# Optimization experiments

Hardware: AMD Instinct MI355X
Metric: run time of the kernel (lower is better)

Reference implementation:

```python
import jax, jax.numpy as jnp
import numpy as np

VOCAB = 200000
EMB = 128
HID = 128
NT = 16
B = 4096


def setup_inputs() -> dict:
    key = jax.random.key(0)
    ks = jax.random.split(key, 8)
    x = jax.random.randint(ks[0], (B, 1), 0, VOCAB, dtype=jnp.int64)
    emb = jax.random.normal(ks[1], (VOCAB, EMB), dtype=jnp.float32) * 0.02
    emb = emb.at[0].set(0.0)  # padding_idx=0
    s = 1.0 / np.sqrt(HID)
    w_ih = jax.random.uniform(ks[2], (4 * HID, EMB), minval=-s, maxval=s, dtype=jnp.float32)
    w_hh = jax.random.uniform(ks[3], (4 * HID, HID), minval=-s, maxval=s, dtype=jnp.float32)
    b_ih = jax.random.uniform(ks[4], (4 * HID,), minval=-s, maxval=s, dtype=jnp.float32)
    b_hh = jax.random.uniform(ks[5], (4 * HID,), minval=-s, maxval=s, dtype=jnp.float32)
    w_fc = jax.random.uniform(ks[6], (NT, HID), minval=-s, maxval=s, dtype=jnp.float32)
    b_fc = jax.random.uniform(ks[7], (NT,), minval=-s, maxval=s, dtype=jnp.float32)
    return {"x": x, "emb": emb, "w_ih": w_ih, "w_hh": w_hh,
            "b_ih": b_ih, "b_hh": b_hh, "w_fc": w_fc, "b_fc": b_fc}


def _lstm(xs, w_ih, w_hh, b_ih, b_hh):
    # xs: [T, E]; torch LSTM with batch=1, gate order i, f, g, o
    H = HID
    b = b_ih + b_hh

    def step(carry, xt):
        h, c = carry
        z = xt @ w_ih.T + h @ w_hh.T + b  # [4H]
        i = jax.nn.sigmoid(z[:H])
        f = jax.nn.sigmoid(z[H:2 * H])
        g = jnp.tanh(z[2 * H:3 * H])
        o = jax.nn.sigmoid(z[3 * H:])
        c = f * c + i * g
        h = o * jnp.tanh(c)
        return (h, c), h

    init = (jnp.zeros((H,), xs.dtype), jnp.zeros((H,), xs.dtype))
    _, hs = jax.lax.scan(step, init, xs)
    return hs  # [T, H]


def reference(x, emb, w_ih, w_hh, b_ih, b_hh, w_fc, b_fc):
    emb = emb.at[0].set(0.0)  # padding_idx=0
    xe = emb[x[:, 0]]  # [B, E] == lstm input viewed as (seq=B, batch=1, E)
    hs = _lstm(xe, w_ih, w_hh, b_ih, b_hh)  # [B, H]
    out = hs @ w_fc.T + b_fc  # [B, NT]; torch .squeeze(1) is a no-op for NT>1
    return out
```

## Files before the change

### kernel.cpp

```cpp
#include <hip/hip_runtime.h>
#include <math.h>

#define EMBD 128
#define HIDD 128
#define NTAR 16
#define BSEQ 4096
#define G4   512
#define CH   8

typedef _Float16 v2h __attribute__((ext_vector_type(2)));

#define DPP_ADD(x, ctrl)                                                     \
    ((x) + __int_as_float(__builtin_amdgcn_update_dpp(                       \
               0, __float_as_int(x), (ctrl), 0xf, 0xf, true)))

__device__ __forceinline__ float fast_sigmoid(float z) {
    return __builtin_amdgcn_rcpf(1.f + __expf(-z));
}
__device__ __forceinline__ float fast_tanh(float z) {
    return 1.f - 2.f * __builtin_amdgcn_rcpf(1.f + __expf(2.f * z));
}

__device__ __forceinline__ v2h pack_f16(float f0, float f1) {
    return __builtin_bit_cast(v2h, __builtin_amdgcn_cvt_pkrtz(f0, f1));
}

__global__ void input_proj_kernel(const int* __restrict__ x,
                                  const float* __restrict__ emb,
                                  const float* __restrict__ w_ih,
                                  const float* __restrict__ b_ih,
                                  const float* __restrict__ b_hh,
                                  float* __restrict__ zxT) {
    const int t = blockIdx.x;
    const int j = threadIdx.x;
    const int u = j >> 2;
    const int g = j & 3;
    const int row = g * HIDD + u;
    const int idx = x[t];
    const float4* __restrict__ er = (const float4*)(emb + (long long)idx * EMBD);
    const float4* __restrict__ wr = (const float4*)(w_ih + row * EMBD);
    float acc = 0.f;
#pragma unroll
    for (int k = 0; k < EMBD / 4; ++k) {
        float4 e = er[k];
        float4 w = wr[k];
        acc += e.x * w.x + e.y * w.y + e.z * w.z + e.w * w.w;
    }
    zxT[(t * HIDD + u) * 4 + g] = acc + b_ih[row] + b_hh[row];
}

__global__ __launch_bounds__(512, 2)
void lstm_seq_kernel(const float* __restrict__ zxT,
                     const float* __restrict__ w_hh,
                     float* __restrict__ hs) {
    __shared__ __align__(16) _Float16 h_db[2][HIDD];

    const int tid = threadIdx.x;
    const int l   = tid & 63;
    const int wv  = tid >> 6;
    const int kq  = l & 3;
    const int us  = l >> 2;
    const int u   = wv * 16 + us;
    const bool writer = (kq == 0);

    v2h w2h[4][16];
#pragma unroll
    for (int g = 0; g < 4; ++g) {
        const float* __restrict__ wr = w_hh + (g * HIDD + u) * HIDD + 32 * kq;
#pragma unroll
        for (int j = 0; j < 4; ++j) {
            const int c0 = 8 * ((j + kq) & 3);
#pragma unroll
            for (int p = 0; p < 4; ++p) {
                const float f0 = wr[c0 + 2 * p];
                const float f1 = wr[c0 + 2 * p + 1];
                w2h[g][4 * j + p] = pack_f16(f0, f1);
            }
        }
    }
#pragma unroll
    for (int g = 0; g < 4; ++g)
#pragma unroll
        for (int k = 0; k < 16; ++k)
            asm volatile("" : "+v"(w2h[g][k]));

    if (tid < HIDD) {
        h_db[0][tid] = (_Float16)0.f;
        h_db[1][tid] = (_Float16)0.f;
    }
    float c = 0.f;
    float hreg[CH];
    float4 zcur[CH];
#pragma unroll
    for (int s = 0; s < CH; ++s) hreg[s] = 0.f;

    const float4* __restrict__ zx4 = (const float4*)zxT;
    __syncthreads();

    for (int tc = 0; tc < BSEQ; tc += CH) {
        if (writer && tc > 0) {
#pragma unroll
            for (int s = 0; s < CH; ++s)
                hs[(tc - CH + s) * HIDD + u] = hreg[s];
        }
#pragma unroll
        for (int s = 0; s < CH; ++s)
            zcur[s] = zx4[(tc + s) * HIDD + u];

#pragma unroll
        for (int s = 0; s < CH; ++s) {
            const uint4* __restrict__ rb =
                (const uint4*)(&h_db[s & 1][32 * kq]);
            const int wb = (s & 1) ^ 1;

            float z0 = 0.f, z1 = 0.f, z2 = 0.f, z3 = 0.f;
#pragma unroll
            for (int j = 0; j < 4; ++j) {
                const int cj = (j + kq) & 3;
                const uint4 hb = rb[cj];
                v2h hp[4];
                hp[0] = __builtin_bit_cast(v2h, hb.x);
                hp[1] = __builtin_bit_cast(v2h, hb.y);
                hp[2] = __builtin_bit_cast(v2h, hb.z);
                hp[3] = __builtin_bit_cast(v2h, hb.w);
#pragma unroll
                for (int p = 0; p < 4; ++p) {
                    z0 = __builtin_amdgcn_fdot2(hp[p], w2h[0][4 * j + p], z0, false);
                    z1 = __builtin_amdgcn_fdot2(hp[p], w2h[1][4 * j + p], z1, false);
                    z2 = __builtin_amdgcn_fdot2(hp[p], w2h[2][4 * j + p], z2, false);
                    z3 = __builtin_amdgcn_fdot2(hp[p], w2h[3][4 * j + p], z3, false);
                }
            }

            z0 = DPP_ADD(z0, 0xB1); z0 = DPP_ADD(z0, 0x4E);
            z1 = DPP_ADD(z1, 0xB1); z1 = DPP_ADD(z1, 0x4E);
            z2 = DPP_ADD(z2, 0xB1); z2 = DPP_ADD(z2, 0x4E);
            z3 = DPP_ADD(z3, 0xB1); z3 = DPP_ADD(z3, 0x4E);

            const float4 zb = zcur[s];
            const float gi = fast_sigmoid(z0 + zb.x);
            const float gf = fast_sigmoid(z1 + zb.y);
            const float gg = fast_tanh   (z2 + zb.z);
            const float go = fast_sigmoid(z3 + zb.w);
            c = gf * c + gi * gg;
            const float h = go * fast_tanh(c);
            hreg[s] = h;
            if (writer) h_db[wb][u] = (_Float16)h;
            __syncthreads();
        }
    }
    if (writer) {
#pragma unroll
        for (int s = 0; s < CH; ++s)
            hs[(BSEQ - CH + s) * HIDD + u] = hreg[s];
    }
}

__global__ void fc_kernel(const float* __restrict__ hs,
                          const float* __restrict__ w_fc,
                          const float* __restrict__ b_fc,
                          float* __restrict__ out) {
    const int gid = blockIdx.x * blockDim.x + threadIdx.x;
    if (gid >= BSEQ * NTAR) return;
    const int n = gid & (NTAR - 1);
    const int t = gid >> 4;
    const float4* __restrict__ hr = (const float4*)(hs + t * HIDD);
    const float4* __restrict__ wr = (const float4*)(w_fc + n * HIDD);
    float acc = 0.f;
#pragma unroll
    for (int k = 0; k < HIDD / 4; ++k) {
        float4 h = hr[k];
        float4 wv = wr[k];
        acc += h.x * wv.x + h.y * wv.y + h.z * wv.z + h.w * wv.w;
    }
    out[gid] = acc + b_fc[n];
}

extern "C" void kernel_launch(void* const* d_in, const int* in_sizes, int n_in,
                              void* d_out, int out_size, void* d_ws, size_t ws_size,
                              hipStream_t stream) {
    const int*   x    = (const int*)d_in[0];
    const float* emb  = (const float*)d_in[1];
    const float* w_ih = (const float*)d_in[2];
    const float* w_hh = (const float*)d_in[3];
    const float* b_ih = (const float*)d_in[4];
    const float* b_hh = (const float*)d_in[5];
    const float* w_fc = (const float*)d_in[6];
    const float* b_fc = (const float*)d_in[7];
    float* out = (float*)d_out;

    float* zxT = (float*)d_ws;
    float* hs  = zxT + (size_t)BSEQ * G4;

    input_proj_kernel<<<BSEQ, G4, 0, stream>>>(x, emb, w_ih, b_ih, b_hh, zxT);
    lstm_seq_kernel<<<1, 512, 0, stream>>>(zxT, w_hh, hs);
    fc_kernel<<<(BSEQ * NTAR + 255) / 256, 256, 0, stream>>>(hs, w_fc, b_fc, out);
}
```

Before: 2.439 ms.

## Distribute gate activations across quad lanes, prefetch next input chunk, split accumulators

Each of the four lanes in a quad now evaluates a single gate activation, selected per lane, using one exp and one rcp with per-lane constants so sigmoid and tanh share a formula. The four results are then broadcast to every lane of the quad with DPP. Input-projection values are loaded as one scalar per lane and prefetched one chunk ahead to hide global load latency in the serial loop. The fdot2 accumulation chains are split into two halves to shorten dependency chains, at the cost of extra selects, DPP moves and registers.

```diff
diff --git a/kernel.cpp b/kernel.cpp
--- a/kernel.cpp
+++ b/kernel.cpp
@@ -13,10 +13,10 @@
 #define DPP_ADD(x, ctrl)                                                     \
     ((x) + __int_as_float(__builtin_amdgcn_update_dpp(                       \
                0, __float_as_int(x), (ctrl), 0xf, 0xf, true)))
-
-__device__ __forceinline__ float fast_sigmoid(float z) {
-    return __builtin_amdgcn_rcpf(1.f + __expf(-z));
-}
+#define DPP_BCAST(x, ctrl)                                                   \
+    (__int_as_float(__builtin_amdgcn_update_dpp(                             \
+         0, __float_as_int(x), (ctrl), 0xf, 0xf, true)))
+
 __device__ __forceinline__ float fast_tanh(float z) {
     return 1.f - 2.f * __builtin_amdgcn_rcpf(1.f + __expf(2.f * z));
 }
@@ -63,6 +63,10 @@
     const int u   = wv * 16 + us;
     const bool writer = (kq == 0);
 
+    const float mA = (kq == 2) ? 2.f : -1.f;
+    const float cA = (kq == 2) ? -2.f : 1.f;
+    const float cB = (kq == 2) ? 1.f : 0.f;
+
     v2h w2h[4][16];
 #pragma unroll
     for (int g = 0; g < 4; ++g) {
@@ -90,11 +94,13 @@
     }
     float c = 0.f;
     float hreg[CH];
-    float4 zcur[CH];
-#pragma unroll
-    for (int s = 0; s < CH; ++s) hreg[s] = 0.f;
-
-    const float4* __restrict__ zx4 = (const float4*)zxT;
+    float zcur[CH], zfut[CH];
+    const int zoff = wv * 64 + l;
+#pragma unroll
+    for (int s = 0; s < CH; ++s) {
+        zcur[s] = zxT[s * G4 + zoff];
+        hreg[s] = 0.f;
+    }
     __syncthreads();
 
     for (int tc = 0; tc < BSEQ; tc += CH) {
@@ -103,9 +109,12 @@
             for (int s = 0; s < CH; ++s)
                 hs[(tc - CH + s) * HIDD + u] = hreg[s];
         }
-#pragma unroll
-        for (int s = 0; s < CH; ++s)
-            zcur[s] = zx4[(tc + s) * HIDD + u];
+        {
+            const int tn = (tc + CH < BSEQ) ? (tc + CH) : (BSEQ - CH);
+#pragma unroll
+            for (int s = 0; s < CH; ++s)
+                zfut[s] = zxT[(tn + s) * G4 + zoff];
+        }
 
 #pragma unroll
         for (int s = 0; s < CH; ++s) {
@@ -113,7 +122,8 @@
                 (const uint4*)(&h_db[s & 1][32 * kq]);
             const int wb = (s & 1) ^ 1;
 
-            float z0 = 0.f, z1 = 0.f, z2 = 0.f, z3 = 0.f;
+            float z0a = 0.f, z1a = 0.f, z2a = 0.f, z3a = 0.f;
+            float z0b = 0.f, z1b = 0.f, z2b = 0.f, z3b = 0.f;
 #pragma unroll
             for (int j = 0; j < 4; ++j) {
                 const int cj = (j + kq) & 3;
@@ -123,31 +133,53 @@
                 hp[1] = __builtin_bit_cast(v2h, hb.y);
                 hp[2] = __builtin_bit_cast(v2h, hb.z);
                 hp[3] = __builtin_bit_cast(v2h, hb.w);
-#pragma unroll
-                for (int p = 0; p < 4; ++p) {
-                    z0 = __builtin_amdgcn_fdot2(hp[p], w2h[0][4 * j + p], z0, false);
-                    z1 = __builtin_amdgcn_fdot2(hp[p], w2h[1][4 * j + p], z1, false);
-                    z2 = __builtin_amdgcn_fdot2(hp[p], w2h[2][4 * j + p], z2, false);
-                    z3 = __builtin_amdgcn_fdot2(hp[p], w2h[3][4 * j + p], z3, false);
+                if (j < 2) {
+#pragma unroll
+                    for (int p = 0; p < 4; ++p) {
+                        z0a = __builtin_amdgcn_fdot2(hp[p], w2h[0][4 * j + p], z0a, false);
+                        z1a = __builtin_amdgcn_fdot2(hp[p], w2h[1][4 * j + p], z1a, false);
+                        z2a = __builtin_amdgcn_fdot2(hp[p], w2h[2][4 * j + p], z2a, false);
+                        z3a = __builtin_amdgcn_fdot2(hp[p], w2h[3][4 * j + p], z3a, false);
+                    }
+                } else {
+#pragma unroll
+                    for (int p = 0; p < 4; ++p) {
+                        z0b = __builtin_amdgcn_fdot2(hp[p], w2h[0][4 * j + p], z0b, false);
+                        z1b = __builtin_amdgcn_fdot2(hp[p], w2h[1][4 * j + p], z1b, false);
+                        z2b = __builtin_amdgcn_fdot2(hp[p], w2h[2][4 * j + p], z2b, false);
+                        z3b = __builtin_amdgcn_fdot2(hp[p], w2h[3][4 * j + p], z3b, false);
+                    }
                 }
             }
+            float z0 = z0a + z0b, z1 = z1a + z1b;
+            float z2 = z2a + z2b, z3 = z3a + z3b;
 
             z0 = DPP_ADD(z0, 0xB1); z0 = DPP_ADD(z0, 0x4E);
             z1 = DPP_ADD(z1, 0xB1); z1 = DPP_ADD(z1, 0x4E);
             z2 = DPP_ADD(z2, 0xB1); z2 = DPP_ADD(z2, 0x4E);
             z3 = DPP_ADD(z3, 0xB1); z3 = DPP_ADD(z3, 0x4E);
 
-            const float4 zb = zcur[s];
-            const float gi = fast_sigmoid(z0 + zb.x);
-            const float gf = fast_sigmoid(z1 + zb.y);
-            const float gg = fast_tanh   (z2 + zb.z);
-            const float go = fast_sigmoid(z3 + zb.w);
+            float zs = z0;
+            zs = (kq == 1) ? z1 : zs;
+            zs = (kq == 2) ? z2 : zs;
+            zs = (kq == 3) ? z3 : zs;
+            const float zfull = zs + zcur[s];
+            const float r   = __builtin_amdgcn_rcpf(1.f + __expf(mA * zfull));
+            const float act = fmaf(cA, r, cB);
+
+            const float gi = DPP_BCAST(act, 0x00);
+            const float gf = DPP_BCAST(act, 0x55);
+            const float gg = DPP_BCAST(act, 0xAA);
+            const float go = DPP_BCAST(act, 0xFF);
+
             c = gf * c + gi * gg;
             const float h = go * fast_tanh(c);
             hreg[s] = h;
             if (writer) h_db[wb][u] = (_Float16)h;
             __syncthreads();
         }
+#pragma unroll
+        for (int s = 0; s < CH; ++s) zcur[s] = zfut[s];
     }
     if (writer) {
 #pragma unroll
```

Measured after the change: 2.367 ms. -3.0%, faster.
